# Performance work log

Hardware: AMD Instinct MI355X
Metric: run time of the kernel (lower is better)

## Reference

```python
import jax, jax.numpy as jnp
import numpy as np

V, E, H, L, B, S = 32000, 512, 512, 2, 32, 128


def setup_inputs() -> dict:
    key = jax.random.key(0)
    ks = jax.random.split(key, 16)
    sc = 0.05
    return {
        "target": jax.random.randint(ks[0], (B, S), 0, V, dtype=jnp.int32),
        "target_length": jax.random.randint(ks[1], (B,), 1, S, dtype=jnp.int32),
        "context": jax.random.normal(ks[2], (L * 2, B, H), jnp.float32) * 0.1,
        "embed_table": jax.random.normal(ks[3], (V, E), jnp.float32) * sc,
        "w_ih0": jax.random.normal(ks[4], (2, 3 * H, E), jnp.float32) * sc,
        "w_hh0": jax.random.normal(ks[5], (2, 3 * H, H), jnp.float32) * sc,
        "b_ih0": jax.random.normal(ks[6], (2, 3 * H), jnp.float32) * sc,
        "b_hh0": jax.random.normal(ks[7], (2, 3 * H), jnp.float32) * sc,
        "w_ih1": jax.random.normal(ks[8], (2, 3 * H, 2 * H), jnp.float32) * sc,
        "w_hh1": jax.random.normal(ks[9], (2, 3 * H, H), jnp.float32) * sc,
        "b_ih1": jax.random.normal(ks[10], (2, 3 * H), jnp.float32) * sc,
        "b_hh1": jax.random.normal(ks[11], (2, 3 * H), jnp.float32) * sc,
        "fc_w": jax.random.normal(ks[12], (V, 2 * H), jnp.float32) * sc,
        "fc_b": jax.random.normal(ks[13], (V,), jnp.float32) * sc,
    }


def _gru_cell(x, h, w_ih, w_hh, b_ih, b_hh):
    # x: [B, in]  h: [2, B, H]  w_ih: [2, 3H, in]  w_hh: [2, 3H, H]
    gi = jnp.einsum('bi,dgi->dbg', x, w_ih) + b_ih[:, None, :]
    gh = jnp.einsum('dbh,dgh->dbg', h, w_hh) + b_hh[:, None, :]
    ir, iz, in_ = jnp.split(gi, 3, axis=-1)
    hr, hz, hn = jnp.split(gh, 3, axis=-1)
    r = jax.nn.sigmoid(ir + hr)
    z = jax.nn.sigmoid(iz + hz)
    n = jnp.tanh(in_ + r * hn)
    return (1.0 - z) * n + z * h  # [2, B, H]


def reference(target, target_length, context, embed_table,
              w_ih0, w_hh0, b_ih0, b_hh0,
              w_ih1, w_hh1, b_ih1, b_hh1,
              fc_w, fc_b):
    b, s = target.shape
    hd = context.shape[-1]
    emb = embed_table[target]                  # [B, S, E] (dropout = identity in eval)
    h0 = context.reshape(L, 2, b, hd)          # torch layout hidden[l*2+d]
    params = [(w_ih0, w_hh0, b_ih0, b_hh0), (w_ih1, w_hh1, b_ih1, b_hh1)]

    def step(h, x_t):                          # h: [L, 2, B, H], x_t: [B, E]
        x = x_t
        new_h = []
        for l in range(L):
            hn = _gru_cell(x, h[l], *params[l])            # [2, B, H]
            new_h.append(hn)
            x = hn.transpose(1, 0, 2).reshape(b, 2 * hd)   # concat fwd|bwd
        return jnp.stack(new_h), x

    _, outs = jax.lax.scan(step, h0, emb.transpose(1, 0, 2))  # outs: [S, B, 2H]
    out = outs.transpose(1, 0, 2)                              # [B, S, 2H]
    logits = jnp.einsum('bsh,vh->bsv', out, fc_w) + fc_b       # [B, S, V]
    return jax.nn.log_softmax(logits, axis=-1)
```

## Files before the change

### kernel.cpp

```cpp
#include <hip/hip_runtime.h>
#include <cstdint>
#include <cstddef>

#define Vv 32000
#define Ee 512
#define Hh 512
#define Bb 32
#define Ss 128

typedef __bf16 bf16x8 __attribute__((ext_vector_type(8)));
typedef float  f32x4  __attribute__((ext_vector_type(4)));
typedef unsigned long long ull;

__device__ __forceinline__ float b2f(unsigned short u) {
  union { unsigned int i; float f; } v; v.i = ((unsigned int)u) << 16; return v.f;
}
__device__ __forceinline__ unsigned short f2b(float f) {
  union { float f; unsigned int i; } v; v.f = f;
  unsigned int r = v.i + 0x7FFFu + ((v.i >> 16) & 1u);
  return (unsigned short)(r >> 16);
}
__device__ __forceinline__ float sigm(float x) { return 1.f / (1.f + __expf(-x)); }

__device__ __forceinline__ ull aload8(const unsigned short* p) {
  return __hip_atomic_load((const ull*)p, __ATOMIC_RELAXED, __HIP_MEMORY_SCOPE_AGENT);
}
__device__ __forceinline__ void astore8(unsigned short* p, ull v) {
  __hip_atomic_store((ull*)p, v, __ATOMIC_RELAXED, __HIP_MEMORY_SCOPE_AGENT);
}


__global__ void zero_flags(unsigned* p) {
  for (int i = threadIdx.x; i < 1024; i += 256) p[i] = 0u;
}

__global__ void cast_bf16(const float* __restrict__ src, unsigned short* __restrict__ dst, int n4) {
  int i = blockIdx.x * 256 + threadIdx.x;
  if (i >= n4) return;
  float4 v = reinterpret_cast<const float4*>(src)[i];
  ushort4 o;
  o.x = f2b(v.x); o.y = f2b(v.y); o.z = f2b(v.z); o.w = f2b(v.w);
  reinterpret_cast<ushort4*>(dst)[i] = o;
}

__global__ void pack_w1(const float* __restrict__ ih, const float* __restrict__ hh,
                        unsigned short* __restrict__ dst) {
  int r = blockIdx.x;
  const float* si = ih + (size_t)r * 1024;
  const float* sh = hh + (size_t)r * 512;
  unsigned short* dr = dst + (size_t)r * 1536;
  for (int c = threadIdx.x; c < 1024; c += 256) dr[c] = f2b(si[c]);
  for (int c = threadIdx.x; c < 512; c += 256) dr[1024 + c] = f2b(sh[c]);
}

__global__ void embed_gather(const int* __restrict__ target, const float* __restrict__ table,
                             unsigned short* __restrict__ emb) {
  int sb = blockIdx.x;
  int s = sb >> 5, b = sb & 31;
  int tok = target[b * Ss + s];
  float4 v = reinterpret_cast<const float4*>(table + (size_t)tok * Ee)[threadIdx.x];
  ushort4 o;
  o.x = f2b(v.x); o.y = f2b(v.y); o.z = f2b(v.z); o.w = f2b(v.w);
  reinterpret_cast<ushort4*>(emb + (size_t)sb * Ee)[threadIdx.x] = o;
}

template <int MODE>
__global__ __launch_bounds__(256, 2) void gemm_nt(
    const unsigned short* __restrict__ A, const unsigned short* __restrict__ Bm,
    const float* __restrict__ bias, void* __restrict__ Cout,
    int K, int ldc, size_t sBz, size_t sCz, size_t sBiasz,
    float* __restrict__ pm, float* __restrict__ ps) {
  int z = blockIdx.z;
  Bm += z * sBz;
  bias += z * sBiasz;

  __shared__ __align__(16) unsigned short As[128 * 64];
  __shared__ __align__(16) unsigned short Bs[128 * 64];
  __shared__ float smx[128][2], sse[128][2];

  int t = threadIdx.x;
  int m0 = blockIdx.x * 128, n0 = blockIdx.y * 128;
  int wave = t >> 6, lane = t & 63;
  int wr = wave >> 1, wc = wave & 1;

  f32x4 acc[4][4] = {};

  int kt = K >> 6;
  for (int ks = 0; ks < kt; ++ks) {
    int k0 = ks << 6;
#pragma unroll
    for (int c = 0; c < 4; ++c) {
      int v = c * 256 + t;
      int row = v >> 3, col = (v & 7) * 8;
      uint4 da = *reinterpret_cast<const uint4*>(A + (size_t)(m0 + row) * K + k0 + col);
      uint4 db = *reinterpret_cast<const uint4*>(Bm + (size_t)(n0 + row) * K + k0 + col);
      *reinterpret_cast<uint4*>(As + v * 8) = da;
      *reinterpret_cast<uint4*>(Bs + v * 8) = db;
    }
    __syncthreads();
#pragma unroll
    for (int kk = 0; kk < 2; ++kk) {
      bf16x8 af[4], bfr[4];
      int lrow = lane & 15, lk = kk * 32 + (lane >> 4) * 8;
#pragma unroll
      for (int m = 0; m < 4; ++m)
        af[m] = *reinterpret_cast<const bf16x8*>(As + (wr * 64 + m * 16 + lrow) * 64 + lk);
#pragma unroll
      for (int n = 0; n < 4; ++n)
        bfr[n] = *reinterpret_cast<const bf16x8*>(Bs + (wc * 64 + n * 16 + lrow) * 64 + lk);
#pragma unroll
      for (int m = 0; m < 4; ++m)
#pragma unroll
        for (int n = 0; n < 4; ++n)
          acc[m][n] = __builtin_amdgcn_mfma_f32_16x16x32_bf16(af[m], bfr[n], acc[m][n], 0, 0, 0);
    }
    __syncthreads();
  }

  int lrow4 = (lane >> 4) * 4, lcol = lane & 15;
  if (MODE == 0) {
#pragma unroll
    for (int m = 0; m < 4; ++m) {
      int rbase = m0 + wr * 64 + m * 16 + lrow4;
#pragma unroll
      for (int n = 0; n < 4; ++n) {
        int col = n0 + wc * 64 + n * 16 + lcol;
        float bv = bias[col];
#pragma unroll
        for (int j = 0; j < 4; ++j) {
          int r = rbase + j;
          float vv = acc[m][n][j] + bv;
          ((unsigned short*)Cout)[z * sCz + (size_t)r * ldc + col] = f2b(vv);
        }
      }
    }
  } else {
    float bv[4];
#pragma unroll
    for (int n = 0; n < 4; ++n) bv[n] = bias[n0 + wc * 64 + n * 16 + lcol];
#pragma unroll
    for (int m = 0; m < 4; ++m) {
#pragma unroll
      for (int j = 0; j < 4; ++j) {
        float x[4];
#pragma unroll
        for (int n = 0; n < 4; ++n) x[n] = acc[m][n][j] + bv[n];
        int rib = wr * 64 + m * 16 + lrow4 + j;
        int r = m0 + rib;
        int b = r & 31, s = r >> 5;
        float* crow = (float*)Cout + (size_t)(b * Ss + s) * ldc;
#pragma unroll
        for (int n = 0; n < 4; ++n)
          __builtin_nontemporal_store(x[n], crow + n0 + wc * 64 + n * 16 + lcol);
        float mx = fmaxf(fmaxf(x[0], x[1]), fmaxf(x[2], x[3]));
#pragma unroll
        for (int msk = 1; msk < 16; msk <<= 1) mx = fmaxf(mx, __shfl_xor(mx, msk, 16));
        float se = __expf(x[0] - mx) + __expf(x[1] - mx) + __expf(x[2] - mx) + __expf(x[3] - mx);
#pragma unroll
        for (int msk = 1; msk < 16; msk <<= 1) se += __shfl_xor(se, msk, 16);
        if (lcol == 0) { smx[rib][wc] = mx; sse[rib][wc] = se; }
      }
    }
    __syncthreads();
    if (t < 128) {
      float ma = smx[t][0], mb = smx[t][1];
      float M = fmaxf(ma, mb);
      float S = sse[t][0] * __expf(ma - M) + sse[t][1] * __expf(mb - M);
      int rg = m0 + t;
      int b = rg & 31, s = rg >> 5;
      size_t orow = (size_t)(b * Ss + s);
      pm[orow * 250 + blockIdx.y] = M;
      ps[orow * 250 + blockIdx.y] = S;
    }
  }
}


#define MFMA16 __builtin_amdgcn_mfma_f32_16x16x32_bf16
#define L1_STRIDE 1544
#define L0_STRIDE 520

__global__ __launch_bounds__(384, 1) void pers_kernel(
    const unsigned short* __restrict__ gi0,
    const unsigned short* __restrict__ whh0b, const unsigned short* __restrict__ w1cat,
    const float* __restrict__ b_hh0, const float* __restrict__ b_ih1, const float* __restrict__ b_hh1,
    const float* __restrict__ context,
    unsigned short* __restrict__ XH, unsigned short* __restrict__ H0,
    unsigned short* __restrict__ outs, unsigned* bar) {
  extern __shared__ __align__(16) unsigned short A_lds[];
  __shared__ float pre[7][16][33];
  __shared__ float hf[32][16];
  __shared__ float bA[16], bB[16], bC[16], bD[16];
  __shared__ unsigned sAbort;

  unsigned* go = bar;
  unsigned* arr = bar + 64;

  const int tid = threadIdx.x, blk = blockIdx.x;

  if (blk == 128) {
    if (tid < 64) {
      for (unsigned v = 1; v <= 130; ++v) {
        ull t0 = __builtin_amdgcn_s_memrealtime();
        bool dead = false;
        while (true) {
          unsigned a0 = __hip_atomic_load(arr + tid * 4, __ATOMIC_RELAXED, __HIP_MEMORY_SCOPE_AGENT);
          unsigned a1 = __hip_atomic_load(arr + (tid + 64) * 4, __ATOMIC_RELAXED, __HIP_MEMORY_SCOPE_AGENT);
          bool ok = (a0 >= v) && (a1 >= v);
          bool to = (__builtin_amdgcn_s_memrealtime() - t0) > 100000000ULL;
          if (__all(ok)) break;
          if (__any(to)) { dead = true; break; }
          __builtin_amdgcn_s_sleep(1);
        }
        if (tid == 0)
          __hip_atomic_store(go, dead ? 0x7FFFFFFFu : v, __ATOMIC_RELAXED, __HIP_MEMORY_SCOPE_AGENT);
        if (dead) return;
      }
    }
    return;
  }

  const int w = tid >> 6, lane = tid & 63, ln = lane & 15;
  const int hi8 = (lane >> 4) * 8;
  const bool isL1 = blk < 64;
  const int d = (blk & 63) >> 5, j0 = (blk & 31) * 16;
  const int g = w >> 1, kh = w & 1;

  auto wait_go = [&](unsigned v) -> bool {
    __syncthreads();
    if (tid == 0) {
      __hip_atomic_store(arr + blk * 4, v, __ATOMIC_RELAXED, __HIP_MEMORY_SCOPE_AGENT);
      ull t0 = __builtin_amdgcn_s_memrealtime();
      unsigned gv;
      while ((gv = __hip_atomic_load(go, __ATOMIC_RELAXED, __HIP_MEMORY_SCOPE_AGENT)) < v) {
        if ((__builtin_amdgcn_s_memrealtime() - t0) > 100000000ULL) {
          gv = 0x7FFFFFFFu;
          __hip_atomic_store(go, gv, __ATOMIC_RELAXED, __HIP_MEMORY_SCOPE_AGENT);
          break;
        }
        __builtin_amdgcn_s_sleep(1);
      }
      sAbort = (gv == 0x7FFFFFFFu) ? 1u : 0u;
    }
    __syncthreads();
    return sAbort != 0u;
  };

  auto stile = [&](int s, f32x4 v0, f32x4 v1) {
    int c = ln, r0 = (lane >> 4) * 4;
#pragma unroll
    for (int j = 0; j < 4; ++j) {
      pre[s][c][r0 + j] = v0[j];
      pre[s][c][16 + r0 + j] = v1[j];
    }
  };

  bf16x8 wreg[24];
  if (isL1) {
    const unsigned short* Bw =
        w1cat + ((size_t)d * 1536 + g * 512 + j0 + ln) * 1536 + kh * 768 + hi8;
#pragma unroll
    for (int i = 0; i < 24; ++i) wreg[i] = *reinterpret_cast<const bf16x8*>(Bw + i * 32);
  } else {
    const unsigned short* Bw =
        whh0b + ((size_t)d * 1536 + g * 512 + j0 + ln) * 512 + kh * 256 + hi8;
#pragma unroll
    for (int i = 0; i < 8; ++i) wreg[i] = *reinterpret_cast<const bf16x8*>(Bw + i * 32);
  }

  if (tid < 16) {
    int jj = tid;
    if (isL1) {
      bA[jj] = b_ih1[d * 1536 + j0 + jj] + b_hh1[d * 1536 + j0 + jj];
      bB[jj] = b_ih1[d * 1536 + 512 + j0 + jj] + b_hh1[d * 1536 + 512 + j0 + jj];
      bC[jj] = b_ih1[d * 1536 + 1024 + j0 + jj];
      bD[jj] = b_hh1[d * 1536 + 1024 + j0 + jj];
    } else {
      bA[jj] = b_hh0[d * 1536 + j0 + jj];
      bB[jj] = b_hh0[d * 1536 + 512 + j0 + jj];
      bC[jj] = b_hh0[d * 1536 + 1024 + j0 + jj];
    }
  }
  {
    int layer = isL1 ? 1 : 0;
    for (int i = tid; i < 128; i += 384) {
      int b = i >> 2, j4 = (i & 3) * 4;
      ull pk = 0;
#pragma unroll
      for (int k = 0; k < 4; ++k) {
        float c = context[(((size_t)layer * 2 + d) * 32 + b) * 512 + j0 + j4 + k];
        hf[b][j4 + k] = c;
        pk |= ((ull)f2b(c)) << (16 * k);
      }
      if (isL1) astore8(XH + (size_t)b * 2048 + 1024 + d * 512 + j0 + j4, pk);
      else      astore8(H0 + (size_t)32768 + ((size_t)d * 32 + b) * 512 + j0 + j4, pk);
    }
  }
  if (wait_go(1)) return;

  for (int p = 0; p <= 128; ++p) {
    ull gr = 0, gz2 = 0, gn2 = 0;

    if (isL1) {
      if (p >= 1) {
        const unsigned short* XHp = XH + (size_t)((p - 1) & 1) * 65536;
        int col = tid * 4;
        int gcol = (col < 1024) ? col : (1024 + d * 512 + (col - 1024));
        const unsigned short* src = XHp + gcol;
        unsigned short* dstl = A_lds + col;
        ull v[32];
#pragma unroll
        for (int b = 0; b < 32; ++b) v[b] = aload8(src + (size_t)b * 2048);
#pragma unroll
        for (int b = 0; b < 32; ++b) *(ull*)(dstl + b * L1_STRIDE) = v[b];
      }
    } else {
      if (p <= 127) {
        if (tid < 128) {
          const unsigned short* gzp =
              gi0 + ((size_t)d * 128 + p) * 32 * 1536 + (size_t)(tid >> 2) * 1536 + j0 + (tid & 3) * 4;
          gr  = *(const ull*)(gzp);
          gz2 = *(const ull*)(gzp + 512);
          gn2 = *(const ull*)(gzp + 1024);
        }
        const unsigned short* H0p =
            H0 + (size_t)((p + 1) & 1) * 32768 + (size_t)d * 32 * 512;
        ull v[11];
#pragma unroll
        for (int k = 0; k < 11; ++k) {
          int idx = tid + k * 384;
          if (idx < 4096) v[k] = aload8(H0p + (size_t)(idx >> 7) * 512 + (idx & 127) * 4);
        }
#pragma unroll
        for (int k = 0; k < 11; ++k) {
          int idx = tid + k * 384;
          if (idx < 4096) *(ull*)(A_lds + (idx >> 7) * L0_STRIDE + (idx & 127) * 4) = v[k];
        }
      }
    }
    __syncthreads();

    if (isL1) {
      if (p >= 1) {
        f32x4 p0 = {}, p1 = {}, q0 = {}, q1 = {};
        const unsigned short* al = A_lds + kh * 768 + hi8;
        if (g == 2 && kh == 1) {
#pragma unroll
          for (int i = 0; i < 8; ++i) {
            bf16x8 a0 = *reinterpret_cast<const bf16x8*>(al + ln * L1_STRIDE + i * 32);
            bf16x8 a1 = *reinterpret_cast<const bf16x8*>(al + (ln + 16) * L1_STRIDE + i * 32);
            p0 = MFMA16(a0, wreg[i], p0, 0, 0, 0);
            p1 = MFMA16(a1, wreg[i], p1, 0, 0, 0);
          }
#pragma unroll
          for (int i = 8; i < 24; ++i) {
            bf16x8 a0 = *reinterpret_cast<const bf16x8*>(al + ln * L1_STRIDE + i * 32);
            bf16x8 a1 = *reinterpret_cast<const bf16x8*>(al + (ln + 16) * L1_STRIDE + i * 32);
            q0 = MFMA16(a0, wreg[i], q0, 0, 0, 0);
            q1 = MFMA16(a1, wreg[i], q1, 0, 0, 0);
          }
          stile(5, p0, p1);
          stile(6, q0, q1);
        } else {
#pragma unroll
          for (int i = 0; i < 24; ++i) {
            bf16x8 a0 = *reinterpret_cast<const bf16x8*>(al + ln * L1_STRIDE + i * 32);
            bf16x8 a1 = *reinterpret_cast<const bf16x8*>(al + (ln + 16) * L1_STRIDE + i * 32);
            p0 = MFMA16(a0, wreg[i], p0, 0, 0, 0);
            p1 = MFMA16(a1, wreg[i], p1, 0, 0, 0);
          }
          stile((g < 2) ? g * 2 + kh : 4, p0, p1);
        }
      }
    } else {
      if (p <= 127) {
        f32x4 p0 = {}, p1 = {};
        const unsigned short* al = A_lds + kh * 256 + hi8;
#pragma unroll
        for (int i = 0; i < 8; ++i) {
          bf16x8 a0 = *reinterpret_cast<const bf16x8*>(al + ln * L0_STRIDE + i * 32);
          bf16x8 a1 = *reinterpret_cast<const bf16x8*>(al + (ln + 16) * L0_STRIDE + i * 32);
          p0 = MFMA16(a0, wreg[i], p0, 0, 0, 0);
          p1 = MFMA16(a1, wreg[i], p1, 0, 0, 0);
        }
        stile((g < 2) ? g * 2 + kh : 4 + kh, p0, p1);
      }
    }
    __syncthreads();

    if (isL1) {
      if (p >= 1 && tid < 128) {
        int t_ = p - 1;
        int b = tid >> 2, j4 = (tid & 3) * 4;
        ull pk = 0;
#pragma unroll
        for (int k = 0; k < 4; ++k) {
          int jj = j4 + k;
          float r = sigm(pre[0][jj][b] + pre[1][jj][b] + bA[jj]);
          float z = sigm(pre[2][jj][b] + pre[3][jj][b] + bB[jj]);
          float nn = tanhf(pre[4][jj][b] + pre[5][jj][b] + bC[jj] +
                           r * (pre[6][jj][b] + bD[jj]));
          float h = hf[b][jj];
          float hnew = (1.f - z) * nn + z * h;
          hf[b][jj] = hnew;
          pk |= ((ull)f2b(hnew)) << (16 * k);
        }
        astore8(XH + (size_t)(p & 1) * 65536 + (size_t)b * 2048 + 1024 + d * 512 + j0 + j4, pk);
        __builtin_nontemporal_store(
            pk, (ull*)(outs + ((size_t)t_ * 32 + b) * 1024 + (size_t)d * 512 + j0 + j4));
      }
    } else {
      if (p <= 127 && tid < 128) {
        int b = tid >> 2, j4 = (tid & 3) * 4;
        int col = j0 + j4;
        ull pk = 0;
#pragma unroll
        for (int k = 0; k < 4; ++k) {
          int jj = j4 + k;
          float gir = b2f((unsigned short)(gr >> (16 * k)));
          float giz = b2f((unsigned short)(gz2 >> (16 * k)));
          float gin = b2f((unsigned short)(gn2 >> (16 * k)));
          float r = sigm(gir + pre[0][jj][b] + pre[1][jj][b] + bA[jj]);
          float z = sigm(giz + pre[2][jj][b] + pre[3][jj][b] + bB[jj]);
          float nn = tanhf(gin + r * (pre[4][jj][b] + pre[5][jj][b] + bC[jj]));
          float h = hf[b][jj];
          float hnew = (1.f - z) * nn + z * h;
          hf[b][jj] = hnew;
          pk |= ((ull)f2b(hnew)) << (16 * k);
        }
        astore8(H0 + (size_t)(p & 1) * 32768 + ((size_t)d * 32 + b) * 512 + col, pk);
        astore8(XH + (size_t)(p & 1) * 65536 + (size_t)b * 2048 + d * 512 + col, pk);
      }
    }
    if (wait_go((unsigned)(p + 2))) return;
  }
}


__global__ __launch_bounds__(128) void lse_reduce(const float* __restrict__ pm,
                                                  const float* __restrict__ ps,
                                                  float* __restrict__ lsebuf) {
  int r = blockIdx.x * 128 + threadIdx.x;
  const float* pmr = pm + (size_t)r * 250;
  const float* psr = ps + (size_t)r * 250;
  float M = -1e30f, S = 0.f;
  for (int i = 0; i < 250; ++i) {
    float m2 = pmr[i], s2 = psr[i];
    if (m2 <= M) {
      S += s2 * __expf(m2 - M);
    } else {
      S = S * __expf(M - m2) + s2;
      M = m2;
    }
  }
  lsebuf[r] = M + __logf(S);
}

__global__ __launch_bounds__(256) void sub_lse(float* __restrict__ out,
                                               const float* __restrict__ lsebuf) {
  int row = blockIdx.x;
  float l = lsebuf[row];
  f32x4* rp = (f32x4*)(out + (size_t)row * Vv);
  for (int i = threadIdx.x; i < 8000; i += 256) {
    f32x4 v = __builtin_nontemporal_load(rp + i);
    v[0] -= l; v[1] -= l; v[2] -= l; v[3] -= l;
    __builtin_nontemporal_store(v, rp + i);
  }
}


extern "C" void kernel_launch(void* const* d_in, const int* in_sizes, int n_in,
                              void* d_out, int out_size, void* d_ws, size_t ws_size,
                              hipStream_t stream) {
  (void)in_sizes; (void)n_in; (void)out_size; (void)ws_size;
  const int*   target  = (const int*)  d_in[0];
  const float* context = (const float*)d_in[2];
  const float* table   = (const float*)d_in[3];
  const float* w_ih0   = (const float*)d_in[4];
  const float* w_hh0   = (const float*)d_in[5];
  const float* b_ih0   = (const float*)d_in[6];
  const float* b_hh0   = (const float*)d_in[7];
  const float* w_ih1   = (const float*)d_in[8];
  const float* w_hh1   = (const float*)d_in[9];
  const float* b_ih1   = (const float*)d_in[10];
  const float* b_hh1   = (const float*)d_in[11];
  const float* fc_w    = (const float*)d_in[12];
  const float* fc_b    = (const float*)d_in[13];
  float* out = (float*)d_out;

  uint8_t* ws = (uint8_t*)d_ws;
  size_t off = 0;
  auto alloc = [&](size_t bytes) {
    uint8_t* p = ws + off;
    off += (bytes + 255) & ~(size_t)255;
    return p;
  };
  unsigned*       bar   = (unsigned*)alloc(4096);
  unsigned short* XH    = (unsigned short*)alloc((size_t)2 * 32 * 2048 * 2);
  unsigned short* H0    = (unsigned short*)alloc((size_t)2 * 2 * 32 * 512 * 2);
  unsigned short* whh0b = (unsigned short*)alloc((size_t)1572864 * 2);
  unsigned short* w1cat = (unsigned short*)alloc((size_t)2 * 1536 * 1536 * 2);
  unsigned short* embb  = (unsigned short*)alloc((size_t)2097152 * 2);
  unsigned short* wih0b = (unsigned short*)alloc((size_t)1572864 * 2);
  unsigned short* gi0   = (unsigned short*)alloc((size_t)12582912 * 2);
  unsigned short* outsb = (unsigned short*)alloc((size_t)4194304 * 2);
  unsigned short* fcwb  = (unsigned short*)alloc((size_t)32768000 * 2);

  float* pm     = (float*)gi0;
  float* ps     = pm + (size_t)4096 * 250;
  float* lsebuf = ps + (size_t)4096 * 250;

  static bool attr_done = false;
  if (!attr_done) {
    hipFuncSetAttribute(reinterpret_cast<const void*>(pers_kernel),
                        hipFuncAttributeMaxDynamicSharedMemorySize, 98816);
    attr_done = true;
  }

  zero_flags<<<dim3(1), 256, 0, stream>>>(bar);
  cast_bf16<<<dim3(1536), 256, 0, stream>>>(w_ih0, wih0b, 393216);
  cast_bf16<<<dim3(1536), 256, 0, stream>>>(w_hh0, whh0b, 393216);
  cast_bf16<<<dim3(32000), 256, 0, stream>>>(fc_w, fcwb, 8192000);
  pack_w1<<<dim3(3072), 256, 0, stream>>>(w_ih1, w_hh1, w1cat);
  embed_gather<<<dim3(4096), 128, 0, stream>>>(target, table, embb);

  gemm_nt<0><<<dim3(32, 12, 2), 256, 0, stream>>>(
      embb, wih0b, b_ih0, gi0, 512, 1536,
      (size_t)1536 * 512, (size_t)4096 * 1536, (size_t)1536, nullptr, nullptr);

  pers_kernel<<<dim3(129), 384, 98816, stream>>>(
      gi0, whh0b, w1cat, b_hh0, b_ih1, b_hh1, context, XH, H0, outsb, bar);

  gemm_nt<1><<<dim3(32, 250, 1), 256, 0, stream>>>(
      outsb, fcwb, fc_b, out, 1024, Vv, 0, 0, 0, pm, ps);

  lse_reduce<<<dim3(32), 128, 0, stream>>>(pm, ps, lsebuf);
  sub_lse<<<dim3(4096), 256, 0, stream>>>(out, lsebuf);
}
```

Before: 1.377 ms.

## Replace central grid barrier with per-block dependency flags and async LDS loads

Drops the coordinator block and its global go/arrive barrier in the persistent GRU kernel. Each block now publishes a per-block progress flag and waits only on the specific producer blocks it depends on, using a 4-deep ring of hidden-state buffers so layers can run up to a few steps out of lockstep. The gi0 prefetch is moved ahead of the wait so its latency overlaps the spin. Separately, the GEMM loads tiles straight into LDS with global_load_lds and the FC GEMM remaps block order for better L2 reuse. These changes add memory-ordering risk because the flags are relaxed atomics without explicit fences.

New measurement: 1.356 ms. No clear change (-1.5%).

```diff
diff --git a/kernel.cpp b/kernel.cpp
--- a/kernel.cpp
+++ b/kernel.cpp
@@ -29,9 +29,15 @@
   __hip_atomic_store((ull*)p, v, __ATOMIC_RELAXED, __HIP_MEMORY_SCOPE_AGENT);
 }
 
+__device__ __forceinline__ void gl_lds16(const unsigned short* g, unsigned short* l) {
+  __builtin_amdgcn_global_load_lds(
+      (const __attribute__((address_space(1))) void*)g,
+      (__attribute__((address_space(3))) void*)l, 16, 0, 0);
+}
+
 
 __global__ void zero_flags(unsigned* p) {
-  for (int i = threadIdx.x; i < 1024; i += 256) p[i] = 0u;
+  for (int i = threadIdx.x; i < 4096; i += 256) p[i] = 0u;
 }
 
 __global__ void cast_bf16(const float* __restrict__ src, unsigned short* __restrict__ dst, int n4) {
@@ -79,7 +85,16 @@
   __shared__ float smx[128][2], sse[128][2];
 
   int t = threadIdx.x;
-  int m0 = blockIdx.x * 128, n0 = blockIdx.y * 128;
+  int bx, by;
+  if (MODE == 1) {
+    int lin = blockIdx.x + (int)gridDim.x * blockIdx.y;
+    int q = (int)(gridDim.x * gridDim.y) >> 3;
+    int wg = (lin & 7) * q + (lin >> 3);
+    bx = wg & 31; by = wg >> 5;
+  } else {
+    bx = blockIdx.x; by = blockIdx.y;
+  }
+  int m0 = bx * 128, n0 = by * 128;
   int wave = t >> 6, lane = t & 63;
   int wr = wave >> 1, wc = wave & 1;
 
@@ -92,10 +107,9 @@
     for (int c = 0; c < 4; ++c) {
       int v = c * 256 + t;
       int row = v >> 3, col = (v & 7) * 8;
-      uint4 da = *reinterpret_cast<const uint4*>(A + (size_t)(m0 + row) * K + k0 + col);
-      uint4 db = *reinterpret_cast<const uint4*>(Bm + (size_t)(n0 + row) * K + k0 + col);
-      *reinterpret_cast<uint4*>(As + v * 8) = da;
-      *reinterpret_cast<uint4*>(Bs + v * 8) = db;
+      int vb = (c * 256 + (t & 192)) * 8;
+      gl_lds16(A + (size_t)(m0 + row) * K + k0 + col, As + vb);
+      gl_lds16(Bm + (size_t)(n0 + row) * K + k0 + col, Bs + vb);
     }
     __syncthreads();
 #pragma unroll
@@ -169,8 +183,8 @@
       int rg = m0 + t;
       int b = rg & 31, s = rg >> 5;
       size_t orow = (size_t)(b * Ss + s);
-      pm[orow * 250 + blockIdx.y] = M;
-      ps[orow * 250 + blockIdx.y] = S;
+      pm[orow * 250 + by] = M;
+      ps[orow * 250 + by] = S;
     }
   }
 }
@@ -193,58 +207,17 @@
   __shared__ float bA[16], bB[16], bC[16], bD[16];
   __shared__ unsigned sAbort;
 
-  unsigned* go = bar;
-  unsigned* arr = bar + 64;
+  unsigned* flags = bar;
+  unsigned* abortf = bar + 3072;
 
   const int tid = threadIdx.x, blk = blockIdx.x;
-
-  if (blk == 128) {
-    if (tid < 64) {
-      for (unsigned v = 1; v <= 130; ++v) {
-        ull t0 = __builtin_amdgcn_s_memrealtime();
-        bool dead = false;
-        while (true) {
-          unsigned a0 = __hip_atomic_load(arr + tid * 4, __ATOMIC_RELAXED, __HIP_MEMORY_SCOPE_AGENT);
-          unsigned a1 = __hip_atomic_load(arr + (tid + 64) * 4, __ATOMIC_RELAXED, __HIP_MEMORY_SCOPE_AGENT);
-          bool ok = (a0 >= v) && (a1 >= v);
-          bool to = (__builtin_amdgcn_s_memrealtime() - t0) > 100000000ULL;
-          if (__all(ok)) break;
-          if (__any(to)) { dead = true; break; }
-          __builtin_amdgcn_s_sleep(1);
-        }
-        if (tid == 0)
-          __hip_atomic_store(go, dead ? 0x7FFFFFFFu : v, __ATOMIC_RELAXED, __HIP_MEMORY_SCOPE_AGENT);
-        if (dead) return;
-      }
-    }
-    return;
-  }
-
   const int w = tid >> 6, lane = tid & 63, ln = lane & 15;
   const int hi8 = (lane >> 4) * 8;
   const bool isL1 = blk < 64;
   const int d = (blk & 63) >> 5, j0 = (blk & 31) * 16;
   const int g = w >> 1, kh = w & 1;
 
-  auto wait_go = [&](unsigned v) -> bool {
-    __syncthreads();
-    if (tid == 0) {
-      __hip_atomic_store(arr + blk * 4, v, __ATOMIC_RELAXED, __HIP_MEMORY_SCOPE_AGENT);
-      ull t0 = __builtin_amdgcn_s_memrealtime();
-      unsigned gv;
-      while ((gv = __hip_atomic_load(go, __ATOMIC_RELAXED, __HIP_MEMORY_SCOPE_AGENT)) < v) {
-        if ((__builtin_amdgcn_s_memrealtime() - t0) > 100000000ULL) {
-          gv = 0x7FFFFFFFu;
-          __hip_atomic_store(go, gv, __ATOMIC_RELAXED, __HIP_MEMORY_SCOPE_AGENT);
-          break;
-        }
-        __builtin_amdgcn_s_sleep(1);
-      }
-      sAbort = (gv == 0x7FFFFFFFu) ? 1u : 0u;
-    }
-    __syncthreads();
-    return sAbort != 0u;
-  };
+  if (tid == 0) sAbort = 0u;
 
   auto stile = [&](int s, f32x4 v0, f32x4 v1) {
     int c = ln, r0 = (lane >> 4) * 4;
@@ -293,17 +266,55 @@
         pk |= ((ull)f2b(c)) << (16 * k);
       }
       if (isL1) astore8(XH + (size_t)b * 2048 + 1024 + d * 512 + j0 + j4, pk);
-      else      astore8(H0 + (size_t)32768 + ((size_t)d * 32 + b) * 512 + j0 + j4, pk);
-    }
-  }
-  if (wait_go(1)) return;
+      else      astore8(H0 + (size_t)3 * 32768 + ((size_t)d * 32 + b) * 512 + j0 + j4, pk);
+    }
+  }
+  __syncthreads();
+  if (tid == 0)
+    __hip_atomic_store(flags + (size_t)blk * 16, 1u, __ATOMIC_RELAXED, __HIP_MEMORY_SCOPE_AGENT);
 
   for (int p = 0; p <= 128; ++p) {
     ull gr = 0, gz2 = 0, gn2 = 0;
+    if (!isL1 && p <= 127 && tid < 128) {
+      const unsigned short* gzp =
+          gi0 + ((size_t)d * 128 + p) * 32 * 1536 + (size_t)(tid >> 2) * 1536 + j0 + (tid & 3) * 4;
+      gr  = *(const ull*)(gzp);
+      gz2 = *(const ull*)(gzp + 512);
+      gn2 = *(const ull*)(gzp + 1024);
+    }
+
+    if (w < 2) {
+      int idx = -1, tgt = 0;
+      if (isL1) {
+        if (w == 0) { if (lane < 64) { idx = 64 + lane; tgt = p + 1; } }
+        else        { if (lane < 32) { idx = d * 32 + lane; tgt = p + 1; } }
+      } else {
+        if (w == 0) { if (lane < 32) { idx = 64 + d * 32 + lane; tgt = p + 1; } }
+        else        { if (lane < 64) { idx = lane; tgt = p - 1; } }
+      }
+      ull t0 = __builtin_amdgcn_s_memrealtime();
+      while (true) {
+        int f = (idx >= 0)
+            ? (int)__hip_atomic_load(flags + (size_t)idx * 16, __ATOMIC_RELAXED, __HIP_MEMORY_SCOPE_AGENT)
+            : 0x7FFFFFF;
+        if (__all(f >= tgt)) break;
+        if ((__builtin_amdgcn_s_memrealtime() - t0) > 100000000ULL ||
+            __hip_atomic_load(abortf, __ATOMIC_RELAXED, __HIP_MEMORY_SCOPE_AGENT) != 0u) {
+          __hip_atomic_store(abortf, 1u, __ATOMIC_RELAXED, __HIP_MEMORY_SCOPE_AGENT);
+          sAbort = 1u;
+          break;
+        }
+        __builtin_amdgcn_s_sleep(1);
+      }
+    }
+    __syncthreads();
+    if (sAbort) return;
+
+    int rs = (p - 1) & 3, wslot = p & 3;
 
     if (isL1) {
       if (p >= 1) {
-        const unsigned short* XHp = XH + (size_t)((p - 1) & 1) * 65536;
+        const unsigned short* XHp = XH + (size_t)rs * 65536;
         int col = tid * 4;
         int gcol = (col < 1024) ? col : (1024 + d * 512 + (col - 1024));
         const unsigned short* src = XHp + gcol;
@@ -316,15 +327,7 @@
       }
     } else {
       if (p <= 127) {
-        if (tid < 128) {
-          const unsigned short* gzp =
-              gi0 + ((size_t)d * 128 + p) * 32 * 1536 + (size_t)(tid >> 2) * 1536 + j0 + (tid & 3) * 4;
-          gr  = *(const ull*)(gzp);
-          gz2 = *(const ull*)(gzp + 512);
-          gn2 = *(const ull*)(gzp + 1024);
-        }
-        const unsigned short* H0p =
-            H0 + (size_t)((p + 1) & 1) * 32768 + (size_t)d * 32 * 512;
+        const unsigned short* H0p = H0 + (size_t)rs * 32768 + (size_t)d * 32 * 512;
         ull v[11];
 #pragma unroll
         for (int k = 0; k < 11; ++k) {
@@ -405,7 +408,7 @@
           hf[b][jj] = hnew;
           pk |= ((ull)f2b(hnew)) << (16 * k);
         }
-        astore8(XH + (size_t)(p & 1) * 65536 + (size_t)b * 2048 + 1024 + d * 512 + j0 + j4, pk);
+        astore8(XH + (size_t)wslot * 65536 + (size_t)b * 2048 + 1024 + d * 512 + j0 + j4, pk);
         __builtin_nontemporal_store(
             pk, (ull*)(outs + ((size_t)t_ * 32 + b) * 1024 + (size_t)d * 512 + j0 + j4));
       }
@@ -428,11 +431,15 @@
           hf[b][jj] = hnew;
           pk |= ((ull)f2b(hnew)) << (16 * k);
         }
-        astore8(H0 + (size_t)(p & 1) * 32768 + ((size_t)d * 32 + b) * 512 + col, pk);
-        astore8(XH + (size_t)(p & 1) * 65536 + (size_t)b * 2048 + d * 512 + col, pk);
-      }
-    }
-    if (wait_go((unsigned)(p + 2))) return;
+        astore8(H0 + (size_t)wslot * 32768 + ((size_t)d * 32 + b) * 512 + col, pk);
+        astore8(XH + (size_t)wslot * 65536 + (size_t)b * 2048 + d * 512 + col, pk);
+      }
+    }
+    __syncthreads();
+    if (tid == 0)
+      __hip_atomic_store(flags + (size_t)blk * 16, (unsigned)(p + 2),
+                         __ATOMIC_RELAXED, __HIP_MEMORY_SCOPE_AGENT);
+    if (!isL1 && p == 127) return;
   }
 }
 
@@ -495,9 +502,9 @@
     off += (bytes + 255) & ~(size_t)255;
     return p;
   };
-  unsigned*       bar   = (unsigned*)alloc(4096);
-  unsigned short* XH    = (unsigned short*)alloc((size_t)2 * 32 * 2048 * 2);
-  unsigned short* H0    = (unsigned short*)alloc((size_t)2 * 2 * 32 * 512 * 2);
+  unsigned*       bar   = (unsigned*)alloc(16384);
+  unsigned short* XH    = (unsigned short*)alloc((size_t)4 * 32 * 2048 * 2);
+  unsigned short* H0    = (unsigned short*)alloc((size_t)4 * 2 * 32 * 512 * 2);
   unsigned short* whh0b = (unsigned short*)alloc((size_t)1572864 * 2);
   unsigned short* w1cat = (unsigned short*)alloc((size_t)2 * 1536 * 1536 * 2);
   unsigned short* embb  = (unsigned short*)alloc((size_t)2097152 * 2);
@@ -528,7 +535,7 @@
       embb, wih0b, b_ih0, gi0, 512, 1536,
       (size_t)1536 * 512, (size_t)4096 * 1536, (size_t)1536, nullptr, nullptr);
 
-  pers_kernel<<<dim3(129), 384, 98816, stream>>>(
+  pers_kernel<<<dim3(128), 384, 98816, stream>>>(
       gi0, whh0b, w1cat, b_hh0, b_ih1, b_hh1, context, XH, H0, outsb, bar);
 
   gemm_nt<1><<<dim3(32, 250, 1), 256, 0, stream>>>(
```
